# Kernel optimization log

Measured on AMD Instinct MI355X. Metric: run time of the kernel, lower is better.

The kernel has to match this reference:

```python
import jax, jax.numpy as jnp
import numpy as np
from jax import lax

DIM = 256
HEADS = 8
DIM_HEAD = 64
INNER = HEADS * DIM_HEAD  # 512
K = 3
PAD = K // 2
KV_STRIDE = 2
SCALE = DIM_HEAD ** -0.5
BN_EPS = 1e-5


def _dw_block(x, w_dw, g, b, m, v, w_pw, stride):
    """depthwise conv -> batchnorm (eval) -> 1x1 conv. x: [B,C,H,W]."""
    c = x.shape[1]
    h = lax.conv_general_dilated(
        x, w_dw, window_strides=(stride, stride),
        padding=[(PAD, PAD), (PAD, PAD)],
        feature_group_count=c,
        dimension_numbers=('NCHW', 'OIHW', 'NCHW'))
    inv = lax.rsqrt(v + BN_EPS)
    h = (h - m[None, :, None, None]) * (g * inv)[None, :, None, None] + b[None, :, None, None]
    return jnp.einsum('oc,bchw->bohw', w_pw, h)


def _heads_flat(t):
    # [B, h*d, H, W] -> [B, h, d, H*W]
    B, hd, H, W = t.shape
    return t.reshape(B, HEADS, DIM_HEAD, H * W)


def _cross_attn(q, k, v, Hq, Wq):
    # q: [B,h,d,i], k/v: [B,h,d,j]
    dots = jnp.einsum('bhdi,bhdj->bhij', q, k) * SCALE
    attn = jax.nn.softmax(dots, axis=-1)
    out = jnp.einsum('bhij,bhdj->bhdi', attn, v)
    B = q.shape[0]
    return out.reshape(B, INNER, Hq, Wq)


def _forward(x, y, q_dw_w, q_bn_gamma, q_bn_beta, q_bn_mean, q_bn_var, q_pw_w,
             kv_dw_w, kv_bn_gamma, kv_bn_beta, kv_bn_mean, kv_bn_var, kv_pw_w,
             out_w, out_b):
    B, _, Hx, Wx = x.shape
    _, _, Hy, Wy = y.shape

    qx = _heads_flat(_dw_block(x, q_dw_w, q_bn_gamma, q_bn_beta, q_bn_mean, q_bn_var, q_pw_w, 1))
    kvx = _dw_block(x, kv_dw_w, kv_bn_gamma, kv_bn_beta, kv_bn_mean, kv_bn_var, kv_pw_w, KV_STRIDE)
    kx, vx = map(_heads_flat, jnp.split(kvx, 2, axis=1))

    qy = _heads_flat(_dw_block(y, q_dw_w, q_bn_gamma, q_bn_beta, q_bn_mean, q_bn_var, q_pw_w, 1))
    kvy = _dw_block(y, kv_dw_w, kv_bn_gamma, kv_bn_beta, kv_bn_mean, kv_bn_var, kv_pw_w, KV_STRIDE)
    ky, vy = map(_heads_flat, jnp.split(kvy, 2, axis=1))

    outx = _cross_attn(qx, ky, vy, Hx, Wx)   # x queries attend to y keys/values
    outy = _cross_attn(qy, kx, vx, Hy, Wy)   # y queries attend to x keys/values

    def proj(o):
        return jnp.einsum('oc,bchw->bohw', out_w, o) + out_b[None, :, None, None]

    return proj(outx), proj(outy)


def setup_inputs() -> dict:
    key = jax.random.key(0)
    ks = jax.random.split(key, 8)
    B, H, W = 8, 32, 32
    return {
        'x': jax.random.normal(ks[0], (B, DIM, H, W), jnp.float32),
        'y': jax.random.normal(ks[1], (B, DIM, H, W), jnp.float32),
        'q_dw_w': jax.random.normal(ks[2], (DIM, 1, K, K), jnp.float32) * 0.1,
        'q_bn_gamma': jnp.ones((DIM,), jnp.float32),
        'q_bn_beta': jnp.zeros((DIM,), jnp.float32),
        'q_bn_mean': jnp.zeros((DIM,), jnp.float32),
        'q_bn_var': jnp.ones((DIM,), jnp.float32),
        'q_pw_w': jax.random.normal(ks[3], (INNER, DIM), jnp.float32) * (DIM ** -0.5),
        'kv_dw_w': jax.random.normal(ks[4], (DIM, 1, K, K), jnp.float32) * 0.1,
        'kv_bn_gamma': jnp.ones((DIM,), jnp.float32),
        'kv_bn_beta': jnp.zeros((DIM,), jnp.float32),
        'kv_bn_mean': jnp.zeros((DIM,), jnp.float32),
        'kv_bn_var': jnp.ones((DIM,), jnp.float32),
        'kv_pw_w': jax.random.normal(ks[5], (2 * INNER, DIM), jnp.float32) * (DIM ** -0.5),
        'out_w': jax.random.normal(ks[6], (DIM, INNER), jnp.float32) * (INNER ** -0.5),
        'out_b': jnp.zeros((DIM,), jnp.float32),
    }


def reference(x, y, q_dw_w, q_bn_gamma, q_bn_beta, q_bn_mean, q_bn_var, q_pw_w,
              kv_dw_w, kv_bn_gamma, kv_bn_beta, kv_bn_mean, kv_bn_var, kv_pw_w,
              out_w, out_b):
    return _forward(x, y, q_dw_w, q_bn_gamma, q_bn_beta, q_bn_mean, q_bn_var, q_pw_w,
                    kv_dw_w, kv_bn_gamma, kv_bn_beta, kv_bn_mean, kv_bn_var, kv_pw_w,
                    out_w, out_b)
```

## Files before the change

### kernel.cpp

```cpp
#include <hip/hip_runtime.h>

#define BN_EPS 1e-5f
#define ATT_SCALE 0.125f

typedef _Float16 half_t;
typedef _Float16 half8 __attribute__((ext_vector_type(8)));
typedef _Float16 half4 __attribute__((ext_vector_type(4)));
typedef float f32x4 __attribute__((ext_vector_type(4)));

__device__ __forceinline__ void gll16(const void* g, void* l) {
    __builtin_amdgcn_global_load_lds((const __attribute__((address_space(1))) void*)g,
                                     (__attribute__((address_space(3))) void*)l, 16, 0, 0);
}

__device__ void prep_body(
    int o, int c,
    const float* qg, const float* qb, const float* qm, const float* qv, const float* qpw,
    const float* kg, const float* kbt, const float* km, const float* kvv, const float* kvpw,
    const float* outw,
    half_t* wq, half_t* wkv, half_t* wout, float* bq, float* bkv, float* red)
{
    if (o >= 1536) {
        int ro = o - 1536;
        #pragma unroll
        for (int ci = 0; ci < 2; ++ci) {
            int cc = ci * 256 + c;
            float wv = outw[(size_t)ro * 512 + cc];
            half_t hh = (half_t)wv;
            wout[(size_t)ro * 1024 + cc]       = hh;
            wout[(size_t)ro * 1024 + 512 + cc] = (half_t)(wv - (float)hh);
        }
        return;
    }
    const float *g, *b, *m, *v, *w; half_t* we; float* be;
    if (o < 512) {
        g = qg; b = qb; m = qm; v = qv;
        w = qpw + (size_t)o * 256; we = wq + (size_t)o * 512; be = bq + o;
    } else {
        int ro = o - 512;
        g = kg; b = kbt; m = km; v = kvv;
        w = kvpw + (size_t)ro * 256; we = wkv + (size_t)ro * 512; be = bkv + ro;
    }
    float s  = g[c] * rsqrtf(v[c] + BN_EPS);
    float tt = b[c] - m[c] * s;
    float wv = w[c];
    float wsv = wv * s;
    half_t hh = (half_t)wsv;
    we[c]       = hh;
    we[256 + c] = (half_t)(wsv - (float)hh);
    float partial = wv * tt;
    #pragma unroll
    for (int off = 32; off > 0; off >>= 1)
        partial += __shfl_down(partial, off, 64);
    if ((c & 63) == 0) red[c >> 6] = partial;
    __syncthreads();
    if (c == 0) *be = red[0] + red[1] + red[2] + red[3];
}

__device__ void dw_body(
    int rp, int img, float* sin,
    const float* x, const float* y,
    const float* qdw, const float* kvdw,
    half_t* qB, half_t* kvB)
{
    const float* in = (img < 8) ? x + (size_t)img * 256 * 1024
                                : y + (size_t)(img - 8) * 256 * 1024;
    int t = threadIdx.x;
    int ch = t & 63, cg = t >> 6;
    int r0 = 2 * rp - 1;
    for (int cc = 0; cc < 4; ++cc) {
        __syncthreads();
        #pragma unroll
        for (int ii = 0; ii < 8; ++ii) {
            int u = ii * 256 + t;
            int sch = u >> 5, row = (u >> 3) & 3, seg = u & 7;
            int gr = r0 + row;
            float4 v4 = {0.f, 0.f, 0.f, 0.f};
            if (gr >= 0 && gr < 32)
                v4 = *(const float4*)(in + (size_t)(cc * 64 + sch) * 1024 + gr * 32 + seg * 4);
            float* d = &sin[sch * 129 + row * 32 + seg * 4];
            d[0] = v4.x; d[1] = v4.y; d[2] = v4.z; d[3] = v4.w;
        }
        __syncthreads();
        int gch = cc * 64 + ch;
        float wq9[9], wk9[9];
        #pragma unroll
        for (int i = 0; i < 9; ++i) { wq9[i] = qdw[gch * 9 + i]; wk9[i] = kvdw[gch * 9 + i]; }
        const float* base = &sin[ch * 129];
        #pragma unroll
        for (int r = 0; r < 2; ++r) {
            #pragma unroll
            for (int c8 = 0; c8 < 8; ++c8) {
                int c = cg * 8 + c8;
                float acc = 0.f;
                #pragma unroll
                for (int dr = 0; dr < 3; ++dr) {
                    const float* rowp = base + (r + dr) * 32;
                    #pragma unroll
                    for (int dc = 0; dc < 3; ++dc) {
                        int cx = c + dc - 1;
                        float pv = (cx >= 0 && cx < 32) ? rowp[cx] : 0.f;
                        acc += wq9[dr * 3 + dc] * pv;
                    }
                }
                half_t hh = (half_t)acc;
                size_t p = (size_t)img * 1024 + (2 * rp + r) * 32 + c;
                qB[p * 512 + gch]       = hh;
                qB[p * 512 + 256 + gch] = (half_t)(acc - (float)hh);
            }
        }
        #pragma unroll
        for (int c4 = 0; c4 < 4; ++c4) {
            int c2 = cg * 4 + c4;
            float acc = 0.f;
            #pragma unroll
            for (int dr = 0; dr < 3; ++dr) {
                const float* rowp = base + dr * 32;
                #pragma unroll
                for (int dc = 0; dc < 3; ++dc) {
                    int cx = 2 * c2 + dc - 1;
                    float pv = (cx >= 0 && cx < 32) ? rowp[cx] : 0.f;
                    acc += wk9[dr * 3 + dc] * pv;
                }
            }
            half_t hh = (half_t)acc;
            size_t p = (size_t)img * 256 + rp * 16 + c2;
            kvB[p * 512 + gch]       = hh;
            kvB[p * 512 + 256 + gch] = (half_t)(acc - (float)hh);
        }
    }
}

__global__ __launch_bounds__(256) void prep_dw_kernel(
    const float* __restrict__ x, const float* __restrict__ y,
    const float* __restrict__ qdw, const float* __restrict__ kvdw,
    const float* __restrict__ qg, const float* __restrict__ qb,
    const float* __restrict__ qm, const float* __restrict__ qv,
    const float* __restrict__ qpw,
    const float* __restrict__ kg, const float* __restrict__ kbt,
    const float* __restrict__ km, const float* __restrict__ kvv,
    const float* __restrict__ kvpw,
    const float* __restrict__ outw,
    half_t* __restrict__ wq, half_t* __restrict__ wkv, half_t* __restrict__ wout,
    float* __restrict__ bq, float* __restrict__ bkv,
    half_t* __restrict__ qB, half_t* __restrict__ kvB)
{
    __shared__ __align__(16) float smem[64 * 129];
    int bx = blockIdx.x;
    if (bx < 256)
        dw_body(bx & 15, bx >> 4, smem, x, y, qdw, kvdw, qB, kvB);
    else
        prep_body(bx - 256, threadIdx.x, qg, qb, qm, qv, qpw,
                  kg, kbt, km, kvv, kvpw, outw, wq, wkv, wout, bq, bkv, smem);
}

template<int MT, int NT, int WGM, int WGN, int KSTEPS, int MODE>
__device__ __forceinline__ void gemm_worker(
    char* lds, const half_t* Ab, const half_t* Bb,
    void* outBuf, const float* bias,
    int K, int NPX, int img, int m0, int n0, float scale)
{
    constexpr int TM = WGM * MT * 16, TN = WGN * NT * 16;
    constexpr int KC = 32 * KSTEPS;
    char* Ah = lds;
    char* Al = lds + TM * KC * 2;
    char* Bh = lds + TM * KC * 4;
    char* Bl = lds + TM * KC * 4 + TN * KC * 2;
    int t = threadIdx.x, w = t >> 6, lane = t & 63, quad = lane >> 4, l15 = lane & 15;
    int wm = w % WGM, wn = w / WGM;
    f32x4 acc[MT][NT] = {};

    for (int kc = 0; kc < K; kc += KC) {
        __syncthreads();
        #pragma unroll
        for (int ii = 0; ii < TM * KSTEPS / 64; ++ii) {
            int u = ii * 256 + t;
            int unit = u >> 6;
            int mt = unit / KSTEPS, ks = unit % KSTEPS;
            int q = (u >> 4) & 3, r = u & 15;
            const half_t* g = Ab + (size_t)(mt * 16 + r) * (2 * K) + kc + ks * 32 + q * 8;
            gll16(g,     Ah + (u & ~63) * 16);
            gll16(g + K, Al + (u & ~63) * 16);
        }
        #pragma unroll
        for (int ii = 0; ii < TN * KSTEPS / 64; ++ii) {
            int u = ii * 256 + t;
            int unit = u >> 6;
            int nt = unit / KSTEPS, ks = unit % KSTEPS;
            int q = (u >> 4) & 3, r = u & 15;
            const half_t* g = Bb + (size_t)(nt * 16 + r) * (2 * K) + kc + ks * 32 + q * 8;
            gll16(g,     Bh + (u & ~63) * 16);
            gll16(g + K, Bl + (u & ~63) * 16);
        }
        __syncthreads();
        #pragma unroll
        for (int ks = 0; ks < KSTEPS; ++ks) {
            half8 afh[MT], afl[MT];
            #pragma unroll
            for (int mi = 0; mi < MT; ++mi) {
                afh[mi] = *(half8*)(Ah + ((wm * MT + mi) * KSTEPS + ks) * 1024 + lane * 16);
                afl[mi] = *(half8*)(Al + ((wm * MT + mi) * KSTEPS + ks) * 1024 + lane * 16);
            }
            #pragma unroll
            for (int ni = 0; ni < NT; ++ni) {
                half8 bh = *(half8*)(Bh + ((wn * NT + ni) * KSTEPS + ks) * 1024 + lane * 16);
                half8 bl = *(half8*)(Bl + ((wn * NT + ni) * KSTEPS + ks) * 1024 + lane * 16);
                #pragma unroll
                for (int mi = 0; mi < MT; ++mi) {
                    acc[mi][ni] = __builtin_amdgcn_mfma_f32_16x16x32_f16(afh[mi], bh, acc[mi][ni], 0, 0, 0);
                    acc[mi][ni] = __builtin_amdgcn_mfma_f32_16x16x32_f16(afh[mi], bl, acc[mi][ni], 0, 0, 0);
                    acc[mi][ni] = __builtin_amdgcn_mfma_f32_16x16x32_f16(afl[mi], bh, acc[mi][ni], 0, 0, 0);
                }
            }
        }
    }

    if (MODE == 2) {
        #pragma unroll
        for (int mi = 0; mi < MT; ++mi) {
            int mrow0 = m0 + wm * MT * 16 + mi * 16 + quad * 4;
            #pragma unroll
            for (int ni = 0; ni < NT; ++ni) {
                int col = n0 + wn * NT * 16 + ni * 16 + l15;
                f32x4 a = acc[mi][ni];
                float* op = (float*)outBuf + (size_t)img * 256 * NPX;
                #pragma unroll
                for (int r = 0; r < 4; ++r)
                    op[(size_t)(mrow0 + r) * NPX + col] = a[r] + bias[mrow0 + r];
            }
        }
    } else {
        __syncthreads();
        float* tbuf = (float*)lds;
        constexpr int TP = 40;
        #pragma unroll
        for (int qtr = 0; qtr < TM / 32; ++qtr) {
            #pragma unroll
            for (int mi = 0; mi < MT; ++mi) {
                int rowblk = wm * MT * 16 + mi * 16;
                if (rowblk >= qtr * 32 && rowblk < qtr * 32 + 32) {
                    int mloc = rowblk - qtr * 32 + quad * 4;
                    #pragma unroll
                    for (int ni = 0; ni < NT; ++ni) {
                        int nloc = wn * NT * 16 + ni * 16 + l15;
                        #pragma unroll
                        for (int r = 0; r < 4; ++r) {
                            float vv = acc[mi][ni][r];
                            if (MODE == 0) vv = (vv + bias[m0 + rowblk + quad * 4 + r]) * scale;
                            else           vv = vv + bias[n0 + nloc];
                            tbuf[nloc * TP + mloc + r] = vv;
                        }
                    }
                }
            }
            __syncthreads();
            #pragma unroll
            for (int it = 0; it < (TN * 4) / 256; ++it) {
                int u = it * 256 + t;
                int n = u >> 2, mg = u & 3;
                float vv[8];
                *(float4*)&vv[0] = *(const float4*)&tbuf[n * TP + mg * 8];
                *(float4*)&vv[4] = *(const float4*)&tbuf[n * TP + mg * 8 + 4];
                half8 hv, lv;
                #pragma unroll
                for (int j = 0; j < 8; ++j) {
                    half_t hh = (half_t)vv[j];
                    hv[j] = hh; lv[j] = (half_t)(vv[j] - (float)hh);
                }
                int mglob = m0 + qtr * 32 + mg * 8;
                if (MODE == 0) {
                    int h = mglob >> 6, d0 = mglob & 63;
                    half_t* op = (half_t*)outBuf + ((size_t)(img * 8 + h) * NPX + n0 + n) * 128 + d0;
                    *(half8*)op = hv;
                    *(half8*)(op + 64) = lv;
                } else {
                    int nn = n0 + n, h = nn >> 6, d = nn & 63;
                    half_t* op = (half_t*)outBuf + ((size_t)(img * 8 + h) * 64 + d) * 512 + mglob;
                    *(half8*)op = hv;
                    *(half8*)(op + 256) = lv;
                }
            }
            __syncthreads();
        }
    }
}

__global__ __launch_bounds__(256) void qkv_kernel(
    const half_t* __restrict__ wq, const half_t* __restrict__ wkv,
    const half_t* __restrict__ qB, const half_t* __restrict__ kvB,
    const float* __restrict__ bq, const float* __restrict__ bkv,
    half_t* __restrict__ qpr, half_t* __restrict__ kpr, half_t* __restrict__ vpr)
{
    __shared__ __align__(16) char lds[32768];
    int tile = blockIdx.x, img = blockIdx.z;
    if (tile < 32) {
        int m0 = (tile >> 3) * 128, n0 = (tile & 7) * 128;
        gemm_worker<4, 4, 2, 2, 1, 0>(lds,
            wq + (size_t)m0 * 512,
            qB + (size_t)img * (1024 * 512) + (size_t)n0 * 512,
            qpr, bq, 256, 1024, img, m0, n0, ATT_SCALE);
    } else if (tile < 40) {
        int tt = tile - 32;
        int m0 = (tt >> 1) * 128, n0 = (tt & 1) * 128;
        gemm_worker<4, 4, 2, 2, 1, 0>(lds,
            wkv + (size_t)m0 * 512,
            kvB + (size_t)img * (256 * 512) + (size_t)n0 * 512,
            kpr, bkv, 256, 256, img, m0, n0, 1.0f);
    } else {
        int tt = tile - 40;
        int m0 = (tt >> 2) * 128, n0 = (tt & 3) * 128;
        gemm_worker<4, 4, 2, 2, 1, 1>(lds,
            kvB + (size_t)img * (256 * 512) + (size_t)m0 * 512,
            wkv + (size_t)(512 + n0) * 512,
            vpr, bkv + 512, 256, 512, img, m0, n0, 1.0f);
    }
}

__global__ __launch_bounds__(256) void out_kernel(
    const half_t* __restrict__ wout, const half_t* __restrict__ attp,
    const float* __restrict__ outb, float* __restrict__ out)
{
    __shared__ __align__(16) char lds[49152];
    int tile = blockIdx.x, img = blockIdx.z;
    int m0 = (tile >> 3) * 64, n0 = (tile & 7) * 128;
    gemm_worker<2, 4, 2, 2, 2, 2>(lds,
        wout + (size_t)m0 * 1024,
        attp + (size_t)img * (1024 * 1024) + (size_t)n0 * 1024,
        out, outb, 512, 1024, img, m0, n0, 1.0f);
}

__global__ __launch_bounds__(512, 4) void attn_fused(
    const half_t* __restrict__ qb, const half_t* __restrict__ kb,
    const half_t* __restrict__ vb, half_t* __restrict__ att)
{
    __shared__ __align__(16) char lds[65536];
    int ic = blockIdx.x, h = blockIdx.y, img = blockIdx.z;
    int partner = img ^ 8;
    int t = threadIdx.x, w = t >> 6, lane = t & 63, quad = lane >> 4, l15 = lane & 15;
    const half_t* qp = qb + ((size_t)(img * 8 + h) * 1024 + ic * 128) * 128;
    const half_t* kp = kb + (size_t)(partner * 8 + h) * 256 * 128;
    const half_t* vp = vb + (size_t)(partner * 8 + h) * 64 * 512;

    half8 qh[2], ql[2];
    #pragma unroll
    for (int kcs = 0; kcs < 2; ++kcs) {
        qh[kcs] = *(const half8*)(qp + (size_t)(w * 16 + l15) * 128 + kcs * 32 + quad * 8);
        ql[kcs] = *(const half8*)(qp + (size_t)(w * 16 + l15) * 128 + 64 + kcs * 32 + quad * 8);
    }

    #pragma unroll
    for (int ii = 0; ii < 4; ++ii) {
        int u = ii * 512 + t;
        const half_t* g = kp + (size_t)((u >> 7) * 16 + (u & 15)) * 128
                             + ((u >> 6) & 1) * 32 + ((u >> 4) & 3) * 8;
        gll16(g,      lds + (u & ~63) * 16);
        gll16(g + 64, lds + 32768 + (u & ~63) * 16);
    }
    __syncthreads();

    f32x4 sacc[16] = {};
    #pragma unroll
    for (int kcs = 0; kcs < 2; ++kcs)
        #pragma unroll
        for (int nt = 0; nt < 16; ++nt) {
            half8 bh = *(const half8*)(lds + (nt * 2 + kcs) * 1024 + lane * 16);
            half8 bl = *(const half8*)(lds + 32768 + (nt * 2 + kcs) * 1024 + lane * 16);
            sacc[nt] = __builtin_amdgcn_mfma_f32_16x16x32_f16(qh[kcs], bh, sacc[nt], 0, 0, 0);
            sacc[nt] = __builtin_amdgcn_mfma_f32_16x16x32_f16(qh[kcs], bl, sacc[nt], 0, 0, 0);
            sacc[nt] = __builtin_amdgcn_mfma_f32_16x16x32_f16(ql[kcs], bh, sacc[nt], 0, 0, 0);
        }

    #pragma unroll
    for (int r = 0; r < 4; ++r) {
        float mx = sacc[0][r];
        #pragma unroll
        for (int nt = 1; nt < 16; ++nt) mx = fmaxf(mx, sacc[nt][r]);
        #pragma unroll
        for (int off = 1; off < 16; off <<= 1) mx = fmaxf(mx, __shfl_xor(mx, off, 64));
        float sum = 0.f;
        #pragma unroll
        for (int nt = 0; nt < 16; ++nt) {
            float e = __expf(sacc[nt][r] - mx);
            sacc[nt][r] = e; sum += e;
        }
        #pragma unroll
        for (int off = 1; off < 16; off <<= 1) sum += __shfl_xor(sum, off, 64);
        float inv = 1.f / sum;
        #pragma unroll
        for (int nt = 0; nt < 16; ++nt) sacc[nt][r] *= inv;
    }
    __syncthreads();

    char* Pw = lds + 16384 + w * 4608;
    f32x4 oacc[4] = {};
    for (int jc = 0; jc < 4; ++jc) {
        #pragma unroll
        for (int n4 = 0; n4 < 4; ++n4)
            #pragma unroll
            for (int r = 0; r < 4; ++r) {
                float pv = sacc[jc * 4 + n4][r];
                half_t hh = (half_t)pv;
                int idx = ((quad * 4 + r) * 72 + n4 * 16 + l15) * 2;
                *(half_t*)(Pw + idx) = hh;
                *(half_t*)(Pw + 2304 + idx) = (half_t)(pv - (float)hh);
            }
        __syncthreads();
        {
            const half_t* g = vp + (size_t)(((t >> 7) & 3) * 16 + (t & 15)) * 512
                                 + jc * 64 + ((t >> 6) & 1) * 32 + ((t >> 4) & 3) * 8;
            gll16(g,       lds + (t & ~63) * 16);
            gll16(g + 256, lds + 8192 + (t & ~63) * 16);
        }
        __syncthreads();
        #pragma unroll
        for (int kcs = 0; kcs < 2; ++kcs) {
            half8 ph = *(const half8*)(Pw + (l15 * 72 + kcs * 32 + quad * 8) * 2);
            half8 pl = *(const half8*)(Pw + 2304 + (l15 * 72 + kcs * 32 + quad * 8) * 2);
            #pragma unroll
            for (int nt = 0; nt < 4; ++nt) {
                half8 vh = *(const half8*)(lds + (nt * 2 + kcs) * 1024 + lane * 16);
                half8 vl = *(const half8*)(lds + 8192 + (nt * 2 + kcs) * 1024 + lane * 16);
                oacc[nt] = __builtin_amdgcn_mfma_f32_16x16x32_f16(ph, vh, oacc[nt], 0, 0, 0);
                oacc[nt] = __builtin_amdgcn_mfma_f32_16x16x32_f16(ph, vl, oacc[nt], 0, 0, 0);
                oacc[nt] = __builtin_amdgcn_mfma_f32_16x16x32_f16(pl, vh, oacc[nt], 0, 0, 0);
            }
        }
    }

    __syncthreads();
    #pragma unroll
    for (int nt = 0; nt < 4; ++nt)
        #pragma unroll
        for (int r = 0; r < 4; ++r) {
            float vv = oacc[nt][r];
            half_t hh = (half_t)vv;
            int row = w * 16 + quad * 4 + r, col = nt * 16 + l15;
            *(half_t*)(lds + (row * 132 + col) * 2) = hh;
            *(half_t*)(lds + (row * 132 + 64 + col) * 2) = (half_t)(vv - (float)hh);
        }
    __syncthreads();
    #pragma unroll
    for (int ii = 0; ii < 4; ++ii) {
        int u = ii * 512 + t;
        int i = u >> 4, seg = (u >> 3) & 1, p8 = u & 7;
        half8 val = *(const half8*)(lds + (i * 132 + seg * 64 + p8 * 8) * 2);
        *(half8*)(att + ((size_t)img * 1024 + ic * 128 + i) * 1024 + seg * 512 + h * 64 + p8 * 8) = val;
    }
}

extern "C" void kernel_launch(void* const* d_in, const int* in_sizes, int n_in,
                              void* d_out, int out_size, void* d_ws, size_t ws_size,
                              hipStream_t stream) {
    const float* x    = (const float*)d_in[0];
    const float* y    = (const float*)d_in[1];
    const float* qdw  = (const float*)d_in[2];
    const float* qg   = (const float*)d_in[3];
    const float* qbb  = (const float*)d_in[4];
    const float* qm   = (const float*)d_in[5];
    const float* qv   = (const float*)d_in[6];
    const float* qpw  = (const float*)d_in[7];
    const float* kvdw = (const float*)d_in[8];
    const float* kg   = (const float*)d_in[9];
    const float* kb_  = (const float*)d_in[10];
    const float* km   = (const float*)d_in[11];
    const float* kvv  = (const float*)d_in[12];
    const float* kvpw = (const float*)d_in[13];
    const float* outw = (const float*)d_in[14];
    const float* outb = (const float*)d_in[15];

    char* ws = (char*)d_ws;
    half_t* wq   = (half_t*)(ws);
    half_t* wkv  = (half_t*)(ws + 524288);
    half_t* wout = (half_t*)(ws + 1572864);
    float*  bq   = (float*) (ws + 2097152);
    float*  bkv  = (float*) (ws + 2099200);
    half_t* qpr  = (half_t*)(ws + 2103296);
    half_t* kpr  = (half_t*)(ws + 35657728);
    half_t* vpr  = (half_t*)(ws + 44046336);
    half_t* qB   = (half_t*)(ws + 52434944);
    half_t* kvB  = (half_t*)(ws + 69212160);
    half_t* attp = (half_t*)(ws + 52434944);

    prep_dw_kernel<<<2048, 256, 0, stream>>>(
        x, y, qdw, kvdw, qg, qbb, qm, qv, qpw, kg, kb_, km, kvv, kvpw, outw,
        wq, wkv, wout, bq, bkv, qB, kvB);

    qkv_kernel<<<dim3(48, 1, 16), 256, 0, stream>>>(
        wq, wkv, qB, kvB, bq, bkv, qpr, kpr, vpr);

    attn_fused<<<dim3(8, 8, 16), 512, 0, stream>>>(qpr, kpr, vpr, attp);

    out_kernel<<<dim3(32, 1, 16), 256, 0, stream>>>(wout, attp, outb, (float*)d_out);
}
```

Before: 231.5 us.

## Double-buffer GEMM and PV loads, pad depthwise LDS, widen QKV blocks

The depthwise conv stage now uses a padded shared-memory tile with zeroed halo columns and loads each thread's row window into registers, which removes the per-tap boundary checks. The GEMM worker switches to double-buffered LDS staging, so the next K chunk is fetched while the current one is consumed. The QKV kernel moves to 512 threads with 64KB of LDS, and occupancy hints are added. In attention, V tiles are prefetched into alternating buffers and the P scratch uses an XOR-swizzled layout to avoid bank conflicts. The larger LDS footprint may reduce occupancy in exchange for the overlap.

```diff
diff --git a/kernel.cpp b/kernel.cpp
--- a/kernel.cpp
+++ b/kernel.cpp
@@ -68,6 +68,11 @@
     int t = threadIdx.x;
     int ch = t & 63, cg = t >> 6;
     int r0 = 2 * rp - 1;
+    #pragma unroll
+    for (int u = t; u < 1024; u += 256) {
+        int c = u >> 4, row = (u >> 2) & 3, pi = u & 3;
+        sin[c * 148 + row * 36 + (pi < 2 ? pi : 32 + pi)] = 0.f;
+    }
     for (int cc = 0; cc < 4; ++cc) {
         __syncthreads();
         #pragma unroll
@@ -78,7 +83,7 @@
             float4 v4 = {0.f, 0.f, 0.f, 0.f};
             if (gr >= 0 && gr < 32)
                 v4 = *(const float4*)(in + (size_t)(cc * 64 + sch) * 1024 + gr * 32 + seg * 4);
-            float* d = &sin[sch * 129 + row * 32 + seg * 4];
+            float* d = &sin[sch * 148 + row * 36 + 2 + seg * 4];
             d[0] = v4.x; d[1] = v4.y; d[2] = v4.z; d[3] = v4.w;
         }
         __syncthreads();
@@ -86,45 +91,40 @@
         float wq9[9], wk9[9];
         #pragma unroll
         for (int i = 0; i < 9; ++i) { wq9[i] = qdw[gch * 9 + i]; wk9[i] = kvdw[gch * 9 + i]; }
-        const float* base = &sin[ch * 129];
+        float rowv[4][12];
+        const float* base = &sin[ch * 148];
+        #pragma unroll
+        for (int rr = 0; rr < 4; ++rr) {
+            *(float4*)&rowv[rr][0] = *(const float4*)(base + rr * 36 + cg * 8);
+            *(float4*)&rowv[rr][4] = *(const float4*)(base + rr * 36 + cg * 8 + 4);
+            *(float4*)&rowv[rr][8] = *(const float4*)(base + rr * 36 + cg * 8 + 8);
+        }
         #pragma unroll
         for (int r = 0; r < 2; ++r) {
             #pragma unroll
             for (int c8 = 0; c8 < 8; ++c8) {
-                int c = cg * 8 + c8;
                 float acc = 0.f;
                 #pragma unroll
-                for (int dr = 0; dr < 3; ++dr) {
-                    const float* rowp = base + (r + dr) * 32;
+                for (int dr = 0; dr < 3; ++dr)
                     #pragma unroll
-                    for (int dc = 0; dc < 3; ++dc) {
-                        int cx = c + dc - 1;
-                        float pv = (cx >= 0 && cx < 32) ? rowp[cx] : 0.f;
-                        acc += wq9[dr * 3 + dc] * pv;
-                    }
-                }
+                    for (int dc = 0; dc < 3; ++dc)
+                        acc += wq9[dr * 3 + dc] * rowv[r + dr][c8 + dc + 1];
                 half_t hh = (half_t)acc;
-                size_t p = (size_t)img * 1024 + (2 * rp + r) * 32 + c;
+                size_t p = (size_t)img * 1024 + (2 * rp + r) * 32 + cg * 8 + c8;
                 qB[p * 512 + gch]       = hh;
                 qB[p * 512 + 256 + gch] = (half_t)(acc - (float)hh);
             }
         }
         #pragma unroll
         for (int c4 = 0; c4 < 4; ++c4) {
-            int c2 = cg * 4 + c4;
             float acc = 0.f;
             #pragma unroll
-            for (int dr = 0; dr < 3; ++dr) {
-                const float* rowp = base + dr * 32;
+            for (int dr = 0; dr < 3; ++dr)
                 #pragma unroll
-                for (int dc = 0; dc < 3; ++dc) {
-                    int cx = 2 * c2 + dc - 1;
-                    float pv = (cx >= 0 && cx < 32) ? rowp[cx] : 0.f;
-                    acc += wk9[dr * 3 + dc] * pv;
-                }
-            }
+                for (int dc = 0; dc < 3; ++dc)
+                    acc += wk9[dr * 3 + dc] * rowv[dr][2 * c4 + dc + 1];
             half_t hh = (half_t)acc;
-            size_t p = (size_t)img * 256 + rp * 16 + c2;
+            size_t p = (size_t)img * 256 + rp * 16 + cg * 4 + c4;
             kvB[p * 512 + gch]       = hh;
             kvB[p * 512 + 256 + gch] = (half_t)(acc - (float)hh);
         }
@@ -145,7 +145,7 @@
     float* __restrict__ bq, float* __restrict__ bkv,
     half_t* __restrict__ qB, half_t* __restrict__ kvB)
 {
-    __shared__ __align__(16) float smem[64 * 129];
+    __shared__ __align__(16) float smem[64 * 148];
     int bx = blockIdx.x;
     if (bx < 256)
         dw_body(bx & 15, bx >> 4, smem, x, y, qdw, kvdw, qB, kvB);
@@ -154,63 +154,65 @@
                   kg, kbt, km, kvv, kvpw, outw, wq, wkv, wout, bq, bkv, smem);
 }
 
-template<int MT, int NT, int WGM, int WGN, int KSTEPS, int MODE>
+template<int MT, int NT, int WGM, int WGN, int NTHR, int MODE>
 __device__ __forceinline__ void gemm_worker(
     char* lds, const half_t* Ab, const half_t* Bb,
     void* outBuf, const float* bias,
     int K, int NPX, int img, int m0, int n0, float scale)
 {
     constexpr int TM = WGM * MT * 16, TN = WGN * NT * 16;
-    constexpr int KC = 32 * KSTEPS;
-    char* Ah = lds;
-    char* Al = lds + TM * KC * 2;
-    char* Bh = lds + TM * KC * 4;
-    char* Bl = lds + TM * KC * 4 + TN * KC * 2;
+    constexpr int BUF = (TM + TN) * 128;
     int t = threadIdx.x, w = t >> 6, lane = t & 63, quad = lane >> 4, l15 = lane & 15;
     int wm = w % WGM, wn = w / WGM;
     f32x4 acc[MT][NT] = {};
-
-    for (int kc = 0; kc < K; kc += KC) {
-        __syncthreads();
-        #pragma unroll
-        for (int ii = 0; ii < TM * KSTEPS / 64; ++ii) {
-            int u = ii * 256 + t;
-            int unit = u >> 6;
-            int mt = unit / KSTEPS, ks = unit % KSTEPS;
-            int q = (u >> 4) & 3, r = u & 15;
-            const half_t* g = Ab + (size_t)(mt * 16 + r) * (2 * K) + kc + ks * 32 + q * 8;
+    const int NC = K / 32;
+
+    auto stage = [&](int kh, int p) {
+        char* Ah = lds + p * BUF;
+        char* Al = Ah + TM * 64;
+        char* Bh = Ah + TM * 128;
+        char* Bl = Bh + TN * 64;
+        #pragma unroll
+        for (int ii = 0; ii < TM * 4 / NTHR; ++ii) {
+            int u = ii * NTHR + t;
+            int mt = u >> 6, q = (u >> 4) & 3, r = u & 15;
+            const half_t* g = Ab + (size_t)(mt * 16 + r) * (2 * K) + kh + q * 8;
             gll16(g,     Ah + (u & ~63) * 16);
             gll16(g + K, Al + (u & ~63) * 16);
         }
         #pragma unroll
-        for (int ii = 0; ii < TN * KSTEPS / 64; ++ii) {
-            int u = ii * 256 + t;
-            int unit = u >> 6;
-            int nt = unit / KSTEPS, ks = unit % KSTEPS;
-            int q = (u >> 4) & 3, r = u & 15;
-            const half_t* g = Bb + (size_t)(nt * 16 + r) * (2 * K) + kc + ks * 32 + q * 8;
+        for (int ii = 0; ii < TN * 4 / NTHR; ++ii) {
+            int u = ii * NTHR + t;
+            int nt = u >> 6, q = (u >> 4) & 3, r = u & 15;
+            const half_t* g = Bb + (size_t)(nt * 16 + r) * (2 * K) + kh + q * 8;
             gll16(g,     Bh + (u & ~63) * 16);
             gll16(g + K, Bl + (u & ~63) * 16);
         }
+    };
+
+    stage(0, 0);
+    for (int kc = 0; kc < NC; ++kc) {
         __syncthreads();
-        #pragma unroll
-        for (int ks = 0; ks < KSTEPS; ++ks) {
-            half8 afh[MT], afl[MT];
+        if (kc + 1 < NC) stage((kc + 1) * 32, (kc + 1) & 1);
+        char* Ah = lds + (kc & 1) * BUF;
+        char* Al = Ah + TM * 64;
+        char* Bh = Ah + TM * 128;
+        char* Bl = Bh + TN * 64;
+        half8 afh[MT], afl[MT];
+        #pragma unroll
+        for (int mi = 0; mi < MT; ++mi) {
+            afh[mi] = *(half8*)(Ah + (wm * MT + mi) * 1024 + lane * 16);
+            afl[mi] = *(half8*)(Al + (wm * MT + mi) * 1024 + lane * 16);
+        }
+        #pragma unroll
+        for (int ni = 0; ni < NT; ++ni) {
+            half8 bh = *(half8*)(Bh + (wn * NT + ni) * 1024 + lane * 16);
+            half8 bl = *(half8*)(Bl + (wn * NT + ni) * 1024 + lane * 16);
             #pragma unroll
             for (int mi = 0; mi < MT; ++mi) {
-                afh[mi] = *(half8*)(Ah + ((wm * MT + mi) * KSTEPS + ks) * 1024 + lane * 16);
-                afl[mi] = *(half8*)(Al + ((wm * MT + mi) * KSTEPS + ks) * 1024 + lane * 16);
-            }
-            #pragma unroll
-            for (int ni = 0; ni < NT; ++ni) {
-                half8 bh = *(half8*)(Bh + ((wn * NT + ni) * KSTEPS + ks) * 1024 + lane * 16);
-                half8 bl = *(half8*)(Bl + ((wn * NT + ni) * KSTEPS + ks) * 1024 + lane * 16);
-                #pragma unroll
-                for (int mi = 0; mi < MT; ++mi) {
-                    acc[mi][ni] = __builtin_amdgcn_mfma_f32_16x16x32_f16(afh[mi], bh, acc[mi][ni], 0, 0, 0);
-                    acc[mi][ni] = __builtin_amdgcn_mfma_f32_16x16x32_f16(afh[mi], bl, acc[mi][ni], 0, 0, 0);
-                    acc[mi][ni] = __builtin_amdgcn_mfma_f32_16x16x32_f16(afl[mi], bh, acc[mi][ni], 0, 0, 0);
-                }
+                acc[mi][ni] = __builtin_amdgcn_mfma_f32_16x16x32_f16(afh[mi], bh, acc[mi][ni], 0, 0, 0);
+                acc[mi][ni] = __builtin_amdgcn_mfma_f32_16x16x32_f16(afh[mi], bl, acc[mi][ni], 0, 0, 0);
+                acc[mi][ni] = __builtin_amdgcn_mfma_f32_16x16x32_f16(afl[mi], bh, acc[mi][ni], 0, 0, 0);
             }
         }
     }
@@ -255,8 +257,8 @@
             }
             __syncthreads();
             #pragma unroll
-            for (int it = 0; it < (TN * 4) / 256; ++it) {
-                int u = it * 256 + t;
+            for (int it = 0; it < (TN * 4) / NTHR; ++it) {
+                int u = it * NTHR + t;
                 int n = u >> 2, mg = u & 3;
                 float vv[8];
                 *(float4*)&vv[0] = *(const float4*)&tbuf[n * TP + mg * 8];
@@ -285,45 +287,45 @@
     }
 }
 
-__global__ __launch_bounds__(256) void qkv_kernel(
+__global__ __launch_bounds__(512, 4) void qkv_kernel(
     const half_t* __restrict__ wq, const half_t* __restrict__ wkv,
     const half_t* __restrict__ qB, const half_t* __restrict__ kvB,
     const float* __restrict__ bq, const float* __restrict__ bkv,
     half_t* __restrict__ qpr, half_t* __restrict__ kpr, half_t* __restrict__ vpr)
 {
-    __shared__ __align__(16) char lds[32768];
+    __shared__ __align__(16) char lds[65536];
     int tile = blockIdx.x, img = blockIdx.z;
     if (tile < 32) {
         int m0 = (tile >> 3) * 128, n0 = (tile & 7) * 128;
-        gemm_worker<4, 4, 2, 2, 1, 0>(lds,
+        gemm_worker<2, 4, 4, 2, 512, 0>(lds,
             wq + (size_t)m0 * 512,
             qB + (size_t)img * (1024 * 512) + (size_t)n0 * 512,
             qpr, bq, 256, 1024, img, m0, n0, ATT_SCALE);
     } else if (tile < 40) {
         int tt = tile - 32;
         int m0 = (tt >> 1) * 128, n0 = (tt & 1) * 128;
-        gemm_worker<4, 4, 2, 2, 1, 0>(lds,
+        gemm_worker<2, 4, 4, 2, 512, 0>(lds,
             wkv + (size_t)m0 * 512,
             kvB + (size_t)img * (256 * 512) + (size_t)n0 * 512,
             kpr, bkv, 256, 256, img, m0, n0, 1.0f);
     } else {
         int tt = tile - 40;
         int m0 = (tt >> 2) * 128, n0 = (tt & 3) * 128;
-        gemm_worker<4, 4, 2, 2, 1, 1>(lds,
+        gemm_worker<2, 4, 4, 2, 512, 1>(lds,
             kvB + (size_t)img * (256 * 512) + (size_t)m0 * 512,
             wkv + (size_t)(512 + n0) * 512,
             vpr, bkv + 512, 256, 512, img, m0, n0, 1.0f);
     }
 }
 
-__global__ __launch_bounds__(256) void out_kernel(
+__global__ __launch_bounds__(256, 3) void out_kernel(
     const half_t* __restrict__ wout, const half_t* __restrict__ attp,
     const float* __restrict__ outb, float* __restrict__ out)
 {
     __shared__ __align__(16) char lds[49152];
     int tile = blockIdx.x, img = blockIdx.z;
     int m0 = (tile >> 3) * 64, n0 = (tile & 7) * 128;
-    gemm_worker<2, 4, 2, 2, 2, 2>(lds,
+    gemm_worker<2, 4, 2, 2, 256, 2>(lds,
         wout + (size_t)m0 * 1024,
         attp + (size_t)img * (1024 * 1024) + (size_t)n0 * 1024,
         out, outb, 512, 1024, img, m0, n0, 1.0f);
@@ -391,7 +393,15 @@
     }
     __syncthreads();
 
-    char* Pw = lds + 16384 + w * 4608;
+    {
+        int u = t;
+        int nt = (u >> 7) & 3, kcs = (u >> 6) & 1, q = (u >> 4) & 3, r = u & 15;
+        const half_t* g = vp + (size_t)(nt * 16 + r) * 512 + kcs * 32 + q * 8;
+        gll16(g,       lds + (u & ~63) * 16);
+        gll16(g + 256, lds + 8192 + (u & ~63) * 16);
+    }
+
+    char* Pw = lds + 32768 + w * 4096;
     f32x4 oacc[4] = {};
     for (int jc = 0; jc < 4; ++jc) {
         #pragma unroll
@@ -400,26 +410,31 @@
             for (int r = 0; r < 4; ++r) {
                 float pv = sacc[jc * 4 + n4][r];
                 half_t hh = (half_t)pv;
-                int idx = ((quad * 4 + r) * 72 + n4 * 16 + l15) * 2;
-                *(half_t*)(Pw + idx) = hh;
-                *(half_t*)(Pw + 2304 + idx) = (half_t)(pv - (float)hh);
+                int row = quad * 4 + r;
+                int cb = (n4 * 16 + l15) * 2;
+                int off = row * 128 + (cb ^ ((row & 7) << 4));
+                *(half_t*)(Pw + off) = hh;
+                *(half_t*)(Pw + 2048 + off) = (half_t)(pv - (float)hh);
             }
         __syncthreads();
-        {
-            const half_t* g = vp + (size_t)(((t >> 7) & 3) * 16 + (t & 15)) * 512
-                                 + jc * 64 + ((t >> 6) & 1) * 32 + ((t >> 4) & 3) * 8;
-            gll16(g,       lds + (t & ~63) * 16);
-            gll16(g + 256, lds + 8192 + (t & ~63) * 16);
-        }
-        __syncthreads();
+        if (jc < 3) {
+            int u = t;
+            int nt = (u >> 7) & 3, kcs = (u >> 6) & 1, q = (u >> 4) & 3, r = u & 15;
+            const half_t* g = vp + (size_t)(nt * 16 + r) * 512 + (jc + 1) * 64 + kcs * 32 + q * 8;
+            char* nb = lds + ((jc + 1) & 1) * 16384;
+            gll16(g,       nb + (u & ~63) * 16);
+            gll16(g + 256, nb + 8192 + (u & ~63) * 16);
+        }
+        char* vbase = lds + (jc & 1) * 16384;
         #pragma unroll
         for (int kcs = 0; kcs < 2; ++kcs) {
-            half8 ph = *(const half8*)(Pw + (l15 * 72 + kcs * 32 + quad * 8) * 2);
-            half8 pl = *(const half8*)(Pw + 2304 + (l15 * 72 + kcs * 32 + quad * 8) * 2);
+            int pofs = (kcs * 64 + quad * 16) ^ ((l15 & 7) << 4);
+            half8 ph = *(const half8*)(Pw + l15 * 128 + pofs);
+            half8 pl = *(const half8*)(Pw + 2048 + l15 * 128 + pofs);
             #pragma unroll
             for (int nt = 0; nt < 4; ++nt) {
-                half8 vh = *(const half8*)(lds + (nt * 2 + kcs) * 1024 + lane * 16);
-                half8 vl = *(const half8*)(lds + 8192 + (nt * 2 + kcs) * 1024 + lane * 16);
+                half8 vh = *(const half8*)(vbase + (nt * 2 + kcs) * 1024 + lane * 16);
+                half8 vl = *(const half8*)(vbase + 8192 + (nt * 2 + kcs) * 1024 + lane * 16);
                 oacc[nt] = __builtin_amdgcn_mfma_f32_16x16x32_f16(ph, vh, oacc[nt], 0, 0, 0);
                 oacc[nt] = __builtin_amdgcn_mfma_f32_16x16x32_f16(ph, vl, oacc[nt], 0, 0, 0);
                 oacc[nt] = __builtin_amdgcn_mfma_f32_16x16x32_f16(pl, vh, oacc[nt], 0, 0, 0);
@@ -485,7 +500,7 @@
         x, y, qdw, kvdw, qg, qbb, qm, qv, qpw, kg, kb_, km, kvv, kvpw, outw,
         wq, wkv, wout, bq, bkv, qB, kvB);
 
-    qkv_kernel<<<dim3(48, 1, 16), 256, 0, stream>>>(
+    qkv_kernel<<<dim3(48, 1, 16), 512, 0, stream>>>(
         wq, wkv, qB, kvB, bq, bkv, qpr, kpr, vpr);
 
     attn_fused<<<dim3(8, 8, 16), 512, 0, stream>>>(qpr, kpr, vpr, attp);
```

Result: faster. 213.2 us (-7.9%).
